# Kernel optimization log

Hardware: AMD Instinct MI355X
Metric: run time of the kernel (lower is better)

The kernel has to match this reference:

```python
import jax, jax.numpy as jnp
import numpy as np
from jax import lax

M = 256        # hidden size (n_h_units)
DIM = 128      # dim_redu, topology feature dim
T = 128        # timesteps
B = 256        # batch
VOCAB = 2000   # number of stored topologies


def setup_inputs() -> dict:
    key = jax.random.key(0)
    ks = jax.random.split(key, 10)
    return {
        "x": jax.random.randint(ks[0], (B,), 0, VOCAB, dtype=jnp.int32),
        "topo": jax.random.normal(ks[1], (VOCAB, T, DIM), dtype=jnp.float32),
        "Wz": jax.random.normal(ks[2], (M, M + DIM), dtype=jnp.float32) * 0.1,
        "Wr": jax.random.normal(ks[3], (M, M + DIM), dtype=jnp.float32) * 0.1,
        "Wh1": jax.random.normal(ks[4], (M, M), dtype=jnp.float32) * 0.1,
        "Wh2": jax.random.normal(ks[5], (M, DIM), dtype=jnp.float32) * 0.1 - 0.1,
        "bz": jax.random.normal(ks[6], (M,), dtype=jnp.float32) * 0.1,
        "br": jax.random.normal(ks[7], (M,), dtype=jnp.float32) * 0.1,
        "bh": jax.random.normal(ks[8], (M,), dtype=jnp.float32) * 0.1,
    }


def reference(x, topo, Wz, Wr, Wh1, Wh2, bz, br, bh):
    # X: [B, T, DIM] -> time-major, feature-major: [T, DIM, B]
    X = jnp.transpose(topo[x], (1, 2, 0))
    # t = 0: h0 = tanh(Wh2 @ x0 + bh)
    h0 = jnp.tanh(Wh2 @ X[0] + bh[:, None])  # [M, B]

    def step(hp, xt):
        # zr = sigmoid(Wzr @ [hp; xt] + bzr), split into update z and reset r
        hx = jnp.concatenate([hp, xt], axis=0)            # [M+DIM, B]
        z = jax.nn.sigmoid(Wz @ hx + bz[:, None])         # [M, B]
        r = jax.nn.sigmoid(Wr @ hx + br[:, None])         # [M, B]
        h_tilde = jnp.tanh(Wh1 @ (r * hp) + Wh2 @ xt + bh[:, None])
        ht = (1.0 - z) * hp + z * h_tilde
        return ht, ht

    _, hs = lax.scan(step, h0, X[1:])                     # hs: [T-1, M, B]
    h_all = jnp.concatenate([h0[None], hs], axis=0)       # [T, M, B]
    # original stacks as [M, T, B] then permutes (2,1,0) -> [B, T, M]
    return jnp.transpose(h_all, (2, 0, 1))
```

## Files before the change

kernel.cpp:

```cpp
#include <hip/hip_runtime.h>
#include <stdint.h>

#define Mh   256
#define DIMx 128
#define Tt   128
#define Bb   256

typedef __attribute__((ext_vector_type(8))) short short8;
typedef __attribute__((ext_vector_type(4))) float f32x4;

static const size_t OFF_GH  = 0;
static const size_t OFF_GL  = 262144;
static const size_t OFF_H1H = 524288;
static const size_t OFF_H1L = 655360;
static const size_t OFF_WXH = 786432;
static const size_t OFF_WXL = 983040;
static const size_t OFF_P   = 1179648;
static const size_t WS_NEED = OFF_P + 3ull*Tt*Bb*Mh*4ull;

__device__ __forceinline__ f32x4 mfma16(short8 a, short8 b, f32x4 c){
  return __builtin_amdgcn_mfma_f32_16x16x32_bf16(a, b, c, 0, 0, 0);
}

__device__ __forceinline__ void split1(float v, uint16_t& hi, uint16_t& lo){
  uint32_t b = __float_as_uint(v);
  hi = (uint16_t)(b >> 16);
  float hf = __uint_as_float(b & 0xFFFF0000u);
  float lf = v - hf;
  lo = (uint16_t)(__float_as_uint(lf) >> 16);
}

__device__ __forceinline__ void split8f(float4 v0, float4 v1, short8& hi, short8& lo){
  float vv[8] = {v0.x, v0.y, v0.z, v0.w, v1.x, v1.y, v1.z, v1.w};
  #pragma unroll
  for (int i = 0; i < 8; ++i){
    uint16_t h, l2; split1(vv[i], h, l2);
    hi[i] = (short)h; lo[i] = (short)l2;
  }
}

__device__ __forceinline__ float sigm(float v){ return 1.0f / (1.0f + __expf(-v)); }
__device__ __forceinline__ float tanhA(float v){
  float e = __expf(2.0f * v);
  return 1.0f - 2.0f / (e + 1.0f);
}

__global__ void prep_kernel(const float* __restrict__ Wz, const float* __restrict__ Wr,
                            const float* __restrict__ Wh1, const float* __restrict__ Wh2,
                            uint8_t* __restrict__ ws){
  int tid = blockIdx.x * 256 + threadIdx.x;
  uint16_t* gh  = (uint16_t*)(ws + OFF_GH);
  uint16_t* gl  = (uint16_t*)(ws + OFF_GL);
  uint16_t* h1h = (uint16_t*)(ws + OFF_H1H);
  uint16_t* h1l = (uint16_t*)(ws + OFF_H1L);
  uint16_t* wxh = (uint16_t*)(ws + OFF_WXH);
  uint16_t* wxl = (uint16_t*)(ws + OFF_WXL);
  if (tid < 16384){
    int l = tid & 63, kt = (tid >> 6) & 7, mt = (tid >> 9) & 15, mat = tid >> 13;
    int c = l & 15, g = l >> 4, m = mt*16 + c, k0 = kt*32 + g*8;
    const float* W = mat ? Wr : Wz;
    #pragma unroll
    for (int i = 0; i < 8; ++i){
      uint16_t h, lo2; split1(W[m*384 + k0 + i], h, lo2);
      gh[(size_t)tid*8 + i] = h; gl[(size_t)tid*8 + i] = lo2;
    }
  } else if (tid < 24576){
    int t2 = tid - 16384;
    int l = t2 & 63, kt = (t2 >> 6) & 7, mt = (t2 >> 9) & 15;
    int c = l & 15, g = l >> 4, m = mt*16 + c, k0 = kt*32 + g*8;
    #pragma unroll
    for (int i = 0; i < 8; ++i){
      uint16_t h, lo2; split1(Wh1[m*256 + k0 + i], h, lo2);
      h1h[(size_t)t2*8 + i] = h; h1l[(size_t)t2*8 + i] = lo2;
    }
  } else if (tid < 36864){
    int t3 = tid - 24576;
    int l = t3 & 63, kt = (t3 >> 6) & 3, mt = (t3 >> 8) & 15, mat = t3 >> 12;
    int c = l & 15, g = l >> 4, m = mt*16 + c, k0 = kt*32 + g*8;
    #pragma unroll
    for (int i = 0; i < 8; ++i){
      int k = k0 + i;
      float v = (mat == 0) ? Wz[m*384 + 256 + k]
              : (mat == 1) ? Wr[m*384 + 256 + k]
                           : Wh2[m*128 + k];
      uint16_t h, lo2; split1(v, h, lo2);
      wxh[(size_t)t3*8 + i] = h; wxl[(size_t)t3*8 + i] = lo2;
    }
  }
}

__launch_bounds__(512, 2)
__global__ void proj_kernel(const int* __restrict__ x, const float* __restrict__ topo,
                            const float* __restrict__ bz, const float* __restrict__ br,
                            const float* __restrict__ bh, const uint8_t* __restrict__ ws,
                            float* __restrict__ P){
  int w = threadIdx.x >> 6, l = threadIdx.x & 63;
  int c = l & 15, g = l >> 4;
  int bt = blockIdx.x & 15, tg = blockIdx.x >> 4;
  int b0 = bt * 16;
  const uint16_t* wxh = (const uint16_t*)(ws + OFF_WXH);
  const uint16_t* wxl = (const uint16_t*)(ws + OFF_WXL);

  short8 BH[3][2][4], BL[3][2][4];
  #pragma unroll
  for (int mat = 0; mat < 3; ++mat)
    #pragma unroll
    for (int mtl = 0; mtl < 2; ++mtl){
      int mt = w*2 + mtl;
      #pragma unroll
      for (int kt = 0; kt < 4; ++kt){
        size_t o = ((((size_t)mat*16 + mt)*4 + kt)*64 + l)*8;
        BH[mat][mtl][kt] = *(const short8*)(wxh + o);
        BL[mat][mtl][kt] = *(const short8*)(wxl + o);
      }
    }
  float bias[3][2];
  #pragma unroll
  for (int mat = 0; mat < 3; ++mat){
    const float* bp = (mat == 0) ? bz : (mat == 1) ? br : bh;
    bias[mat][0] = bp[(w*2 + 0)*16 + c];
    bias[mat][1] = bp[(w*2 + 1)*16 + c];
  }
  int64_t tbase = (int64_t)x[b0 + (l & 15)] * (Tt * DIMx);

  for (int tt = 0; tt < 8; ++tt){
    int t = tg*8 + tt;
    const float* xp = topo + tbase + (int64_t)t * DIMx;
    f32x4 acc[3][2];
    #pragma unroll
    for (int mat = 0; mat < 3; ++mat)
      #pragma unroll
      for (int mtl = 0; mtl < 2; ++mtl){
        f32x4 a; a[0] = a[1] = a[2] = a[3] = bias[mat][mtl]; acc[mat][mtl] = a;
      }
    #pragma unroll
    for (int kt = 0; kt < 4; ++kt){
      float4 v0 = *(const float4*)(xp + kt*32 + g*8);
      float4 v1 = *(const float4*)(xp + kt*32 + g*8 + 4);
      short8 ahi, alo; split8f(v0, v1, ahi, alo);
      #pragma unroll
      for (int mat = 0; mat < 3; ++mat)
        #pragma unroll
        for (int mtl = 0; mtl < 2; ++mtl){
          acc[mat][mtl] = mfma16(ahi, BH[mat][mtl][kt], acc[mat][mtl]);
          acc[mat][mtl] = mfma16(ahi, BL[mat][mtl][kt], acc[mat][mtl]);
          acc[mat][mtl] = mfma16(alo, BH[mat][mtl][kt], acc[mat][mtl]);
        }
    }
    #pragma unroll
    for (int mat = 0; mat < 3; ++mat)
      #pragma unroll
      for (int mtl = 0; mtl < 2; ++mtl){
        int m0 = (w*2 + mtl)*16;
        #pragma unroll
        for (int i = 0; i < 4; ++i){
          P[(((size_t)mat*Tt + t)*Bb + (b0 + 4*g + i))*Mh + m0 + c] = acc[mat][mtl][i];
        }
      }
  }
}

__launch_bounds__(512, 2)
__global__ void gru_kernel(const uint8_t* __restrict__ ws, const float* __restrict__ P,
                           float* __restrict__ out){
  extern __shared__ uint8_t lds[];
  const int tx = threadIdx.x;
  const int w = tx >> 6, l = tx & 63;
  const int c = l & 15, g = l >> 4;
  const int b0 = blockIdx.x * 16;
  const uint16_t* gh  = (const uint16_t*)(ws + OFF_GH);
  const uint16_t* gl  = (const uint16_t*)(ws + OFF_GL);
  const uint16_t* h1h = (const uint16_t*)(ws + OFF_H1H);
  const uint16_t* h1l = (const uint16_t*)(ws + OFF_H1L);
  const float* Pz = P;
  const float* Pr = P + (size_t)Tt*Bb*Mh;
  const float* Ph = P + 2*(size_t)Tt*Bb*Mh;

  short8 GH[2][2][8];
  #pragma unroll
  for (int mat = 0; mat < 2; ++mat)
    #pragma unroll
    for (int mtl = 0; mtl < 2; ++mtl)
      #pragma unroll
      for (int kt = 0; kt < 8; ++kt){
        size_t o = ((((size_t)mat*16 + (w*2 + mtl))*8 + kt)*64 + l)*8;
        GH[mat][mtl][kt] = *(const short8*)(gh + o);
      }
  short8 H1H7[2];
  #pragma unroll
  for (int mtl = 0; mtl < 2; ++mtl){
    size_t o = (((size_t)(w*2 + mtl)*8 + 7)*64 + l)*8;
    H1H7[mtl] = *(const short8*)(h1h + o);
  }
  for (int f = w; f < 112; f += 8){
    int mt = f / 7, kt = f % 7;
    float4 v = *(const float4*)(h1h + (((size_t)mt*8 + kt)*64 + l)*8);
    *(float4*)(lds + ((size_t)(mt*7 + kt)*64 + l)*16) = v;
  }
  __syncthreads();

  const int HOFF = 114688, SOFF = 131072;
  const int r = c;
  const int aswz = (r & 7) << 4;
  const int swA0 = ((r*1024 + g*32) ^ aswz);
  const int swA1 = ((r*1024 + g*32 + 16) ^ aswz);

  #pragma unroll
  for (int mtl = 0; mtl < 2; ++mtl){
    int m0 = (w*2 + mtl)*16;
    #pragma unroll
    for (int i = 0; i < 4; ++i){
      int brow = 4*g + i;
      float v = Ph[((size_t)0*Bb + (b0 + brow))*Mh + m0 + c];
      float h0 = tanhA(v);
      int ad = ((brow*1024 + (m0 + c)*4) ^ ((brow & 7) << 4));
      *(float*)(lds + HOFF + ad) = h0;
      out[(size_t)(b0 + brow)*Tt*Mh + m0 + c] = h0;
    }
  }
  __syncthreads();

  for (int t = 1; t < Tt; ++t){
    f32x4 accZ[2], accR[2];
    #pragma unroll
    for (int mtl = 0; mtl < 2; ++mtl){
      int m0 = (w*2 + mtl)*16;
      #pragma unroll
      for (int i = 0; i < 4; ++i){
        size_t pi = (((size_t)t)*Bb + (b0 + 4*g + i))*Mh + m0 + c;
        accZ[mtl][i] = Pz[pi];
        accR[mtl][i] = Pr[pi];
      }
    }
    #pragma unroll
    for (int kt = 0; kt < 8; ++kt){
      float4 v0 = *(const float4*)(lds + HOFF + swA0 + kt*128);
      float4 v1 = *(const float4*)(lds + HOFF + swA1 + kt*128);
      short8 ahi, alo; split8f(v0, v1, ahi, alo);
      #pragma unroll
      for (int mtl = 0; mtl < 2; ++mtl){
        int mt = w*2 + mtl;
        short8 zlo = *(const short8*)(gl + ((((size_t)0*16 + mt)*8 + kt)*64 + l)*8);
        short8 rlo = *(const short8*)(gl + ((((size_t)1*16 + mt)*8 + kt)*64 + l)*8);
        accZ[mtl] = mfma16(ahi, GH[0][mtl][kt], accZ[mtl]);
        accZ[mtl] = mfma16(ahi, zlo,            accZ[mtl]);
        accZ[mtl] = mfma16(alo, GH[0][mtl][kt], accZ[mtl]);
        accR[mtl] = mfma16(ahi, GH[1][mtl][kt], accR[mtl]);
        accR[mtl] = mfma16(ahi, rlo,            accR[mtl]);
        accR[mtl] = mfma16(alo, GH[1][mtl][kt], accR[mtl]);
      }
    }
    float zv[2][4], hpv[2][4];
    #pragma unroll
    for (int mtl = 0; mtl < 2; ++mtl){
      int m0 = (w*2 + mtl)*16;
      #pragma unroll
      for (int i = 0; i < 4; ++i){
        int brow = 4*g + i;
        int ad = ((brow*1024 + (m0 + c)*4) ^ ((brow & 7) << 4));
        float hp = *(const float*)(lds + HOFF + ad);
        float z  = sigm(accZ[mtl][i]);
        float rr = sigm(accR[mtl][i]);
        zv[mtl][i] = z; hpv[mtl][i] = hp;
        *(float*)(lds + SOFF + ad) = rr * hp;
      }
    }
    __syncthreads();
    f32x4 accH[2];
    #pragma unroll
    for (int mtl = 0; mtl < 2; ++mtl){
      int m0 = (w*2 + mtl)*16;
      #pragma unroll
      for (int i = 0; i < 4; ++i)
        accH[mtl][i] = Ph[(((size_t)t)*Bb + (b0 + 4*g + i))*Mh + m0 + c];
    }
    #pragma unroll
    for (int kt = 0; kt < 8; ++kt){
      float4 v0 = *(const float4*)(lds + SOFF + swA0 + kt*128);
      float4 v1 = *(const float4*)(lds + SOFF + swA1 + kt*128);
      short8 shi, slo; split8f(v0, v1, shi, slo);
      #pragma unroll
      for (int mtl = 0; mtl < 2; ++mtl){
        int mt = w*2 + mtl;
        short8 whi = (kt < 7) ? *(const short8*)(lds + ((size_t)(mt*7 + kt)*64 + l)*16)
                              : H1H7[mtl];
        short8 wlo = *(const short8*)(h1l + (((size_t)mt*8 + kt)*64 + l)*8);
        accH[mtl] = mfma16(shi, whi, accH[mtl]);
        accH[mtl] = mfma16(shi, wlo, accH[mtl]);
        accH[mtl] = mfma16(slo, whi, accH[mtl]);
      }
    }
    #pragma unroll
    for (int mtl = 0; mtl < 2; ++mtl){
      int m0 = (w*2 + mtl)*16;
      #pragma unroll
      for (int i = 0; i < 4; ++i){
        int brow = 4*g + i;
        float ht = tanhA(accH[mtl][i]);
        float hn = hpv[mtl][i] + zv[mtl][i] * (ht - hpv[mtl][i]);
        int ad = ((brow*1024 + (m0 + c)*4) ^ ((brow & 7) << 4));
        *(float*)(lds + HOFF + ad) = hn;
        out[(size_t)(b0 + brow)*Tt*Mh + (size_t)t*Mh + m0 + c] = hn;
      }
    }
    __syncthreads();
  }
}

extern "C" void kernel_launch(void* const* d_in, const int* in_sizes, int n_in,
                              void* d_out, int out_size, void* d_ws, size_t ws_size,
                              hipStream_t stream){
  const int*   x    = (const int*)  d_in[0];
  const float* topo = (const float*)d_in[1];
  const float* Wz   = (const float*)d_in[2];
  const float* Wr   = (const float*)d_in[3];
  const float* Wh1  = (const float*)d_in[4];
  const float* Wh2  = (const float*)d_in[5];
  const float* bz   = (const float*)d_in[6];
  const float* br   = (const float*)d_in[7];
  const float* bh   = (const float*)d_in[8];
  uint8_t* ws = (uint8_t*)d_ws;
  float*   P  = (float*)(ws + OFF_P);
  float*   out = (float*)d_out;

  if (ws_size < WS_NEED){
    hipMemsetAsync(d_out, 0, (size_t)out_size * sizeof(float), stream);
    return;
  }
  hipFuncSetAttribute((const void*)gru_kernel,
                      hipFuncAttributeMaxDynamicSharedMemorySize, 147456);

  prep_kernel<<<144, 256, 0, stream>>>(Wz, Wr, Wh1, Wh2, ws);
  proj_kernel<<<256, 512, 0, stream>>>(x, topo, bz, br, bh, ws, P);
  gru_kernel<<<16, 512, 147456, stream>>>(ws, P, out);
}
```

Baseline: 1.715 ms.

## Prefetch next-step projections, pre-split r*h into bf16 LDS, pin weight registers

The GRU recurrence now loads the next timestep's Pz/Pr/Ph projections one iteration ahead, so global-load latency overlaps the current step's MFMA work. The r*h product is split into bf16 hi/lo halves once when written to LDS, and the B operands are read back directly instead of reloading floats and re-splitting them per kt. Empty asm constraints keep weight fragments in VGPRs, and the launch bounds become explicit waves-per-EU attributes. The trade-off is higher register pressure from the prefetch buffers and extra 16-bit LDS stores.

```diff
diff --git a/kernel.cpp b/kernel.cpp
--- a/kernel.cpp
+++ b/kernel.cpp
@@ -89,7 +89,7 @@
   }
 }
 
-__launch_bounds__(512, 2)
+__attribute__((amdgpu_flat_work_group_size(512,512), amdgpu_waves_per_eu(2,2)))
 __global__ void proj_kernel(const int* __restrict__ x, const float* __restrict__ topo,
                             const float* __restrict__ bz, const float* __restrict__ br,
                             const float* __restrict__ bh, const uint8_t* __restrict__ ws,
@@ -114,6 +114,15 @@
         BL[mat][mtl][kt] = *(const short8*)(wxl + o);
       }
     }
+  #pragma unroll
+  for (int mat = 0; mat < 3; ++mat)
+    #pragma unroll
+    for (int mtl = 0; mtl < 2; ++mtl)
+      #pragma unroll
+      for (int kt = 0; kt < 4; ++kt){
+        asm volatile("" : "+v"(BH[mat][mtl][kt]));
+        asm volatile("" : "+v"(BL[mat][mtl][kt]));
+      }
   float bias[3][2];
   #pragma unroll
   for (int mat = 0; mat < 3; ++mat){
@@ -160,7 +169,7 @@
   }
 }
 
-__launch_bounds__(512, 2)
+__attribute__((amdgpu_flat_work_group_size(512,512), amdgpu_waves_per_eu(2,2)))
 __global__ void gru_kernel(const uint8_t* __restrict__ ws, const float* __restrict__ P,
                            float* __restrict__ out){
   extern __shared__ uint8_t lds[];
@@ -192,6 +201,16 @@
     size_t o = (((size_t)(w*2 + mtl)*8 + 7)*64 + l)*8;
     H1H7[mtl] = *(const short8*)(h1h + o);
   }
+  #pragma unroll
+  for (int mat = 0; mat < 2; ++mat)
+    #pragma unroll
+    for (int mtl = 0; mtl < 2; ++mtl)
+      #pragma unroll
+      for (int kt = 0; kt < 8; ++kt)
+        asm volatile("" : "+v"(GH[mat][mtl][kt]));
+  asm volatile("" : "+v"(H1H7[0]));
+  asm volatile("" : "+v"(H1H7[1]));
+
   for (int f = w; f < 112; f += 8){
     int mt = f / 7, kt = f % 7;
     float4 v = *(const float4*)(h1h + (((size_t)mt*8 + kt)*64 + l)*8);
@@ -199,15 +218,27 @@
   }
   __syncthreads();
 
-  const int HOFF = 114688, SOFF = 131072;
+  const int HOFF = 114688, SHI = 131072, SLO = 139264;
   const int r = c;
-  const int aswz = (r & 7) << 4;
-  const int swA0 = ((r*1024 + g*32) ^ aswz);
-  const int swA1 = ((r*1024 + g*32 + 16) ^ aswz);
-
+  const int swzA = (r & 7) << 4;
+  const int hA0 = HOFF + ((r*1024 + g*32) ^ swzA);
+  const int hA1 = HOFF + ((r*1024 + g*32 + 16) ^ swzA);
+  const int m0w = w*32;
+
+  float pzn[2][4], prn[2][4], phn[2][4];
   #pragma unroll
   for (int mtl = 0; mtl < 2; ++mtl){
-    int m0 = (w*2 + mtl)*16;
+    int m0 = m0w + mtl*16;
+    #pragma unroll
+    for (int i = 0; i < 4; ++i){
+      size_t pi = ((size_t)1*Bb + (b0 + 4*g + i))*Mh + m0 + c;
+      pzn[mtl][i] = Pz[pi]; prn[mtl][i] = Pr[pi]; phn[mtl][i] = Ph[pi];
+    }
+  }
+
+  #pragma unroll
+  for (int mtl = 0; mtl < 2; ++mtl){
+    int m0 = m0w + mtl*16;
     #pragma unroll
     for (int i = 0; i < 4; ++i){
       int brow = 4*g + i;
@@ -222,20 +253,29 @@
 
   for (int t = 1; t < Tt; ++t){
     f32x4 accZ[2], accR[2];
+    float phc[2][4];
+    #pragma unroll
+    for (int mtl = 0; mtl < 2; ++mtl)
+      #pragma unroll
+      for (int i = 0; i < 4; ++i){
+        accZ[mtl][i] = pzn[mtl][i];
+        accR[mtl][i] = prn[mtl][i];
+        phc[mtl][i]  = phn[mtl][i];
+      }
+    int tn = (t < Tt-1) ? t+1 : Tt-1;
     #pragma unroll
     for (int mtl = 0; mtl < 2; ++mtl){
-      int m0 = (w*2 + mtl)*16;
+      int m0 = m0w + mtl*16;
       #pragma unroll
       for (int i = 0; i < 4; ++i){
-        size_t pi = (((size_t)t)*Bb + (b0 + 4*g + i))*Mh + m0 + c;
-        accZ[mtl][i] = Pz[pi];
-        accR[mtl][i] = Pr[pi];
+        size_t pi = ((size_t)tn*Bb + (b0 + 4*g + i))*Mh + m0 + c;
+        pzn[mtl][i] = Pz[pi]; prn[mtl][i] = Pr[pi]; phn[mtl][i] = Ph[pi];
       }
     }
     #pragma unroll
     for (int kt = 0; kt < 8; ++kt){
-      float4 v0 = *(const float4*)(lds + HOFF + swA0 + kt*128);
-      float4 v1 = *(const float4*)(lds + HOFF + swA1 + kt*128);
+      float4 v0 = *(const float4*)(lds + hA0 + kt*128);
+      float4 v1 = *(const float4*)(lds + hA1 + kt*128);
       short8 ahi, alo; split8f(v0, v1, ahi, alo);
       #pragma unroll
       for (int mtl = 0; mtl < 2; ++mtl){
@@ -253,53 +293,55 @@
     float zv[2][4], hpv[2][4];
     #pragma unroll
     for (int mtl = 0; mtl < 2; ++mtl){
-      int m0 = (w*2 + mtl)*16;
+      int m0 = m0w + mtl*16;
       #pragma unroll
       for (int i = 0; i < 4; ++i){
         int brow = 4*g + i;
-        int ad = ((brow*1024 + (m0 + c)*4) ^ ((brow & 7) << 4));
-        float hp = *(const float*)(lds + HOFF + ad);
+        int adf = ((brow*1024 + (m0 + c)*4) ^ ((brow & 7) << 4));
+        int adh = ((brow*512  + (m0 + c)*2) ^ ((brow & 7) << 4));
+        float hp = *(const float*)(lds + HOFF + adf);
         float z  = sigm(accZ[mtl][i]);
         float rr = sigm(accR[mtl][i]);
         zv[mtl][i] = z; hpv[mtl][i] = hp;
-        *(float*)(lds + SOFF + ad) = rr * hp;
+        float s = rr * hp;
+        uint16_t shi, slo2; split1(s, shi, slo2);
+        *(uint16_t*)(lds + SHI + adh) = shi;
+        *(uint16_t*)(lds + SLO + adh) = slo2;
       }
     }
     __syncthreads();
     f32x4 accH[2];
     #pragma unroll
-    for (int mtl = 0; mtl < 2; ++mtl){
-      int m0 = (w*2 + mtl)*16;
+    for (int mtl = 0; mtl < 2; ++mtl)
       #pragma unroll
       for (int i = 0; i < 4; ++i)
-        accH[mtl][i] = Ph[(((size_t)t)*Bb + (b0 + 4*g + i))*Mh + m0 + c];
-    }
+        accH[mtl][i] = phc[mtl][i];
     #pragma unroll
     for (int kt = 0; kt < 8; ++kt){
-      float4 v0 = *(const float4*)(lds + SOFF + swA0 + kt*128);
-      float4 v1 = *(const float4*)(lds + SOFF + swA1 + kt*128);
-      short8 shi, slo; split8f(v0, v1, shi, slo);
+      int so = ((r*512 + kt*64 + g*16) ^ swzA);
+      short8 shi8 = *(const short8*)(lds + SHI + so);
+      short8 slo8 = *(const short8*)(lds + SLO + so);
       #pragma unroll
       for (int mtl = 0; mtl < 2; ++mtl){
         int mt = w*2 + mtl;
         short8 whi = (kt < 7) ? *(const short8*)(lds + ((size_t)(mt*7 + kt)*64 + l)*16)
                               : H1H7[mtl];
         short8 wlo = *(const short8*)(h1l + (((size_t)mt*8 + kt)*64 + l)*8);
-        accH[mtl] = mfma16(shi, whi, accH[mtl]);
-        accH[mtl] = mfma16(shi, wlo, accH[mtl]);
-        accH[mtl] = mfma16(slo, whi, accH[mtl]);
+        accH[mtl] = mfma16(shi8, whi, accH[mtl]);
+        accH[mtl] = mfma16(shi8, wlo, accH[mtl]);
+        accH[mtl] = mfma16(slo8, whi, accH[mtl]);
       }
     }
     #pragma unroll
     for (int mtl = 0; mtl < 2; ++mtl){
-      int m0 = (w*2 + mtl)*16;
+      int m0 = m0w + mtl*16;
       #pragma unroll
       for (int i = 0; i < 4; ++i){
         int brow = 4*g + i;
         float ht = tanhA(accH[mtl][i]);
         float hn = hpv[mtl][i] + zv[mtl][i] * (ht - hpv[mtl][i]);
-        int ad = ((brow*1024 + (m0 + c)*4) ^ ((brow & 7) << 4));
-        *(float*)(lds + HOFF + ad) = hn;
+        int adf = ((brow*1024 + (m0 + c)*4) ^ ((brow & 7) << 4));
+        *(float*)(lds + HOFF + adf) = hn;
         out[(size_t)(b0 + brow)*Tt*Mh + (size_t)t*Mh + m0 + c] = hn;
       }
     }
```

Result: slower. 2.108 ms (+22.9%).
